# Optimization experiments

Hardware: AMD Instinct MI355X
Metric: run time of the kernel (lower is better)

Reference implementation:

```python
import jax, jax.numpy as jnp
import numpy as np

NEG = -1e30  # stand-in for -inf that keeps logaddexp grad-safe


def _ctc_neg_log_likelihood(predictions, labels):
    # predictions: [B, T, C] logits; labels: [B, L] int, -1 = padding.
    # tf.nn.ctc_loss(blank_index=-1) => blank class is C-1.
    B, T, C = predictions.shape
    L = labels.shape[1]
    S = 2 * L + 1
    blank = C - 1

    label_len = jnp.sum((labels != -1).astype(jnp.int32), axis=-1)  # [B]
    labels_c = jnp.where(labels < 0, 0, labels).astype(jnp.int32)

    # Extended label sequence: blank, l1, blank, l2, ..., blank  -> [B, S]
    ext = jnp.full((B, S), blank, dtype=jnp.int32)
    ext = ext.at[:, 1::2].set(labels_c)

    # s-2 transition allowed only at label positions (odd s) with ext[s] != ext[s-2]
    same = jnp.concatenate([jnp.zeros((B, 2), bool), ext[:, 2:] == ext[:, :-2]], axis=1)
    is_label_pos = (jnp.arange(S) % 2 == 1)[None, :]
    allow2 = is_label_pos & ~same  # [B, S]

    # valid extended positions per example: s < 2*label_len + 1
    valid = jnp.arange(S)[None, :] < (2 * label_len + 1)[:, None]  # [B, S]

    log_probs = jax.nn.log_softmax(predictions, axis=-1)  # [B, T, C]
    # emission log-prob for each extended-label slot: [B, T, S]
    lp_ext = jnp.take_along_axis(log_probs, jnp.broadcast_to(ext[:, None, :], (B, T, S)), axis=2)

    has_lab = label_len > 0
    alpha0 = jnp.full((B, S), NEG, dtype=log_probs.dtype)
    alpha0 = alpha0.at[:, 0].set(lp_ext[:, 0, 0])
    alpha0 = alpha0.at[:, 1].set(jnp.where(has_lab, lp_ext[:, 0, 1], NEG))
    alpha0 = jnp.where(valid, alpha0, NEG)

    def step(alpha, lp_t):
        a1 = alpha
        a2 = jnp.pad(alpha, ((0, 0), (1, 0)), constant_values=NEG)[:, :S]
        a3 = jnp.pad(alpha, ((0, 0), (2, 0)), constant_values=NEG)[:, :S]
        a3 = jnp.where(allow2, a3, NEG)
        new = jnp.logaddexp(jnp.logaddexp(a1, a2), a3) + lp_t
        new = jnp.where(valid, new, NEG)
        return new, None

    lp_rest = jnp.moveaxis(lp_ext[:, 1:], 1, 0)  # [T-1, B, S]
    alphaT, _ = jax.lax.scan(step, alpha0, lp_rest)

    idx1 = (2 * label_len)[:, None]              # final blank
    idx2 = jnp.maximum(idx1 - 1, 0)              # final label
    a_end1 = jnp.take_along_axis(alphaT, idx1, axis=1)[:, 0]
    a_end2 = jnp.take_along_axis(alphaT, idx2, axis=1)[:, 0]
    a_end2 = jnp.where(has_lab, a_end2, NEG)
    log_lik = jnp.logaddexp(a_end1, a_end2)
    return -log_lik  # [B]


def setup_inputs() -> dict:
    key = jax.random.key(0)
    k1, k2 = jax.random.split(key)
    B, T, C, L = 1024, 384, 96, 48
    labels = jax.random.randint(k1, (B, L), 0, C - 1).astype(jnp.int64)
    predictions = jax.random.normal(k2, (B, T, C), dtype=jnp.float32)
    return {"labels": labels, "predictions": predictions}


def reference(labels, predictions):
    per_example = _ctc_neg_log_likelihood(predictions, labels)
    return jnp.mean(per_example)
```

## Files before the change

kernel.cpp:

```cpp
#include <hip/hip_runtime.h>

constexpr int Tt = 384;
constexpr int Cc = 96;
constexpr int Ll = 48;
constexpr int Gg = 8;
constexpr int NG = 24;

#define L2E 1.4426950408889634f
#define LN2 0.6931471805599453f
#define LNEG (-3.0e38f)

template <int CTRL, int RM = 0xF>
__device__ __forceinline__ float dppf(float x) {
    return __int_as_float(
        __builtin_amdgcn_update_dpp(0, __float_as_int(x), CTRL, RM, 0xF, true));
}
template <int CTRL>
__device__ __forceinline__ int dppi(int x) {
    return __builtin_amdgcn_update_dpp(0, x, CTRL, 0xF, 0xF, true);
}
__device__ __forceinline__ float bcast63(float x) {
    return __int_as_float(__builtin_amdgcn_readlane(__float_as_int(x), 63));
}
__device__ __forceinline__ float wsum(float x) {
    x += dppf<0x111>(x);
    x += dppf<0x112>(x);
    x += dppf<0x114>(x);
    x += dppf<0x118>(x);
    x += dppf<0x142, 0xA>(x);
    x += dppf<0x143, 0xC>(x);
    return bcast63(x);
}
__device__ __forceinline__ float shup1(float x) { return dppf<0x138>(x); }
__device__ __forceinline__ float shdn1(float x) { return dppf<0x130>(x); }
__device__ __forceinline__ float exp2i(int d) {
    d = d < -126 ? -126 : (d > 126 ? 126 : d);
    return __int_as_float((d + 127) << 23);
}

template <bool FWD>
__device__ __forceinline__ void half_pass(const float2* __restrict__ rp2, int lane,
                                          int idx_h, int bitsel, float allow2f,
                                          float& st_e, float& st_o, int& ls) {
    float2 q[Gg];
    float pbC[Gg], plC[Gg], pbN[Gg], plN[Gg];

    auto loadg = [&](int g) {
#pragma unroll
        for (int j = 0; j < Gg; ++j) {
            int k = g * Gg + j;
            int t = FWD ? k : (Tt - 1 - k);
            q[j] = (lane < 48) ? rp2[(size_t)t * 48 + lane] : make_float2(-1e4f, -1e4f);
        }
    };
    auto emit = [&](float* pb, float* pl, int gnext) {
        float ex[Gg], ey[Gg], s[Gg], gb[Gg], g0[Gg], g1[Gg];
#pragma unroll
        for (int j = 0; j < Gg; ++j) {
            ex[j] = exp2f(q[j].x * L2E);
            ey[j] = exp2f(q[j].y * L2E);
            s[j]  = ex[j] + ey[j];
        }
#pragma unroll
        for (int j = 0; j < Gg; ++j) {
            gb[j] = __shfl(ey[j], 47, 64);
            g0[j] = __shfl(ex[j], idx_h, 64);
            g1[j] = __shfl(ey[j], idx_h, 64);
        }
        if (gnext < NG) loadg(gnext);
#pragma unroll
        for (int j = 0; j < Gg; ++j) s[j] = wsum(s[j]);
#pragma unroll
        for (int j = 0; j < Gg; ++j) {
            float rZ = __builtin_amdgcn_rcpf(s[j]);
            pb[j] = gb[j] * rZ;
            pl[j] = (bitsel ? g1[j] : g0[j]) * rZ;
        }
    };

    float f   = 1.0f;
    float a2f = allow2f;

    loadg(0);
    emit(pbC, plC, 1);

    for (int g = 0; g < NG; ++g) {
        if (g + 1 < NG) emit(pbN, plN, g + 2);
#pragma unroll
        for (int j = 0; j < Gg; ++j) {
            if (FWD) {
                float sh = shup1(st_o);
                float t0 = st_e + st_o;
                float ne = fmaf(f, sh, st_e) * pbC[j];
                float no = fmaf(a2f, sh, t0) * plC[j];
                st_e = ne; st_o = no;
            } else {
                float en = shdn1(st_e);
                float on = shdn1(st_o);
                float ne = (st_e + st_o) * pbC[j];
                float no = fmaf(a2f, on, fmaf(f, en, st_o)) * plC[j];
                st_e = ne; st_o = no;
            }
        }
        float m = fmaxf(st_e, st_o);
        bool z = (m == 0.0f);
        int eb = (__float_as_int(m) >> 23) & 0xFF;
        eb = eb > 253 ? 253 : eb;
        float r = z ? 1.0f : __int_as_float((254 - eb) << 23);
        st_e *= r; st_o *= r;
        ls += z ? 0 : (eb - 127);
#pragma unroll
        for (int it = 0; it < 8; ++it) {
            int lsn = FWD ? dppi<0x138>(ls) : dppi<0x130>(ls);
            ls = z ? lsn : ls;
        }
        int lsn2 = FWD ? dppi<0x138>(ls) : dppi<0x130>(ls);
        f = exp2i(lsn2 - ls);
        a2f = allow2f * f;
        if (g + 1 < NG) {
#pragma unroll
            for (int j = 0; j < Gg; ++j) { pbC[j] = pbN[j]; plC[j] = plN[j]; }
        }
    }
}

__global__ __launch_bounds__(64) void zero_kernel(float* o) { *o = 0.0f; }

__global__ __launch_bounds__(128) void ctc_fb(const int* __restrict__ labels,
                                              const float* __restrict__ pred,
                                              float* __restrict__ out,
                                              float invB) {
    const int b    = blockIdx.x;
    const int lane = threadIdx.x & 63;
    const int wv   = threadIdx.x >> 6;
    const float2* rp2 = (const float2*)(pred + (size_t)b * Tt * Cc);

    int v = (lane < Ll) ? labels[(size_t)b * Ll + lane] : -1;
    int present = (lane < Ll) && (v != -1);
    int labv = (v < 0) ? 0 : v;
    unsigned long long pm = __ballot(present);
    int len = __popcll(pm);

    int idx_h  = labv >> 1;
    int bitsel = labv & 1;
    int lab_p = __shfl(labv, (lane - 1) & 63, 64);
    int lab_n = __shfl(labv, (lane + 1) & 63, 64);

    __shared__ float sbe[64], sbo[64];
    __shared__ int   slsb[64];

    float Ae = 0.0f, Ao = 0.0f;
    int ls_f = 0;
    if (wv == 0) {
        float allow2f = (lane >= 1 && labv != lab_p) ? 1.0f : 0.0f;
        float a_e = (lane == 0) ? 1.0f : 0.0f;
        float a_o = 0.0f;
        half_pass<true>(rp2, lane, idx_h, bitsel, allow2f, a_e, a_o, ls_f);
        float sh  = shup1(a_o);
        int   lsu = dppi<0x138>(ls_f);
        float fup = exp2i(lsu - ls_f);
        Ae = fmaf(fup, sh, a_e);
        Ao = fmaf(allow2f * fup, sh, a_e + a_o);
    } else {
        float allow2f = (labv != lab_n) ? 1.0f : 0.0f;
        float b_e = (lane == len) ? 1.0f : 0.0f;
        float b_o = 0.0f;
        int ls_b = 0;
        half_pass<false>(rp2, lane, idx_h, bitsel, allow2f, b_e, b_o, ls_b);
        sbe[lane]  = b_e;
        sbo[lane]  = b_o;
        slsb[lane] = ls_b;
    }
    __syncthreads();

    if (wv == 0) {
        float be = sbe[lane], bo = sbo[lane];
        float base = (float)(ls_f + slsb[lane]);
        float l1 = (Ae > 0.0f && be > 0.0f) ? __log2f(Ae) + __log2f(be) + base : LNEG;
        float l2 = (Ao > 0.0f && bo > 0.0f) ? __log2f(Ao) + __log2f(bo) + base : LNEG;
        float mm = fmaxf(l1, l2);
#pragma unroll
        for (int off = 32; off >= 1; off >>= 1) mm = fmaxf(mm, __shfl_xor(mm, off, 64));
        float ss = exp2f(l1 - mm) + exp2f(l2 - mm);
#pragma unroll
        for (int off = 32; off >= 1; off >>= 1) ss += __shfl_xor(ss, off, 64);
        if (lane == 0) {
            float ll = (mm + __log2f(ss)) * LN2;
            atomicAdd(out, -ll * invB);
        }
    }
}

extern "C" void kernel_launch(void* const* d_in, const int* in_sizes, int n_in,
                              void* d_out, int out_size, void* d_ws, size_t ws_size,
                              hipStream_t stream) {
    const int*   labels = (const int*)d_in[0];
    const float* pred   = (const float*)d_in[1];
    float*       out    = (float*)d_out;

    const int B = in_sizes[0] / Ll;

    hipLaunchKernelGGL(zero_kernel, dim3(1), dim3(64), 0, stream, out);
    hipLaunchKernelGGL(ctc_fb, dim3(B), dim3(128), 0, stream,
                       labels, pred, out, 1.0f / (float)B);
}
```

Baseline: 227.2 us.

## Split emission softmax into separate kernel writing fp16 probs to workspace

Adds a preceding kernel that computes softmax-normalised emission probabilities for each extended-label slot with 8 waves per example, and stores them as fp16 into a [B,T,64] workspace. Lane 48 holds the blank probability. The recurrence kernel then only loads the precomputed halves with a four-group prefetch and broadcasts the blank value via readlane. This removes the exp/shuffle/reduction work from the serial recurrence critical path and cuts the bytes it reads. In exchange it adds a workspace round trip and a second launch, and fp16 storage of probabilities risks precision loss or underflow for small values.

Measured after the change: 248.1 us. 1.09x slower.

```diff
diff --git a/kernel.cpp b/kernel.cpp
--- a/kernel.cpp
+++ b/kernel.cpp
@@ -1,10 +1,12 @@
 #include <hip/hip_runtime.h>
+#include <hip/hip_fp16.h>
 
 constexpr int Tt = 384;
 constexpr int Cc = 96;
 constexpr int Ll = 48;
 constexpr int Gg = 8;
 constexpr int NG = 24;
+constexpr int ES = 64;
 
 #define L2E 1.4426950408889634f
 #define LN2 0.6931471805599453f
@@ -38,54 +40,83 @@
     return __int_as_float((d + 127) << 23);
 }
 
+__global__ __launch_bounds__(512) void emit_kernel(const int* __restrict__ labels,
+                                                   const float* __restrict__ pred,
+                                                   __half* __restrict__ em,
+                                                   float* __restrict__ out) {
+    const int b    = blockIdx.x;
+    const int lane = threadIdx.x & 63;
+    const int wv   = threadIdx.x >> 6;
+    if (b == 0 && threadIdx.x == 0) *out = 0.0f;
+
+    const float2* rp2  = (const float2*)(pred + (size_t)b * Tt * Cc);
+    __half*       erow = em + (size_t)b * Tt * ES;
+
+    int v = (lane < Ll) ? labels[(size_t)b * Ll + lane] : 0;
+    int labv   = (v < 0) ? 0 : v;
+    int idx_h  = labv >> 1;
+    int bitsel = labv & 1;
+
+    constexpr int U = 4;
+    for (int base = wv; base < Tt; base += 8 * U) {
+        float2 q[U];
+#pragma unroll
+        for (int u = 0; u < U; ++u) {
+            int t = base + 8 * u;
+            q[u] = (lane < 48) ? rp2[(size_t)t * 48 + lane] : make_float2(-1e4f, -1e4f);
+        }
+#pragma unroll
+        for (int u = 0; u < U; ++u) {
+            float ex = exp2f(q[u].x * L2E);
+            float ey = exp2f(q[u].y * L2E);
+            float s  = (lane < 48) ? (ex + ey) : 0.0f;
+            float gb = __shfl(ey, 47, 64);
+            float g0 = __shfl(ex, idx_h, 64);
+            float g1 = __shfl(ey, idx_h, 64);
+            s = wsum(s);
+            float rZ = __builtin_amdgcn_rcpf(s);
+            float pl = (bitsel ? g1 : g0) * rZ;
+            float pb = gb * rZ;
+            float val = (lane < 48) ? pl : pb;
+            int t = base + 8 * u;
+            erow[(size_t)t * ES + lane] = __float2half(val);
+        }
+    }
+}
+
 template <bool FWD>
-__device__ __forceinline__ void half_pass(const float2* __restrict__ rp2, int lane,
-                                          int idx_h, int bitsel, float allow2f,
-                                          float& st_e, float& st_o, int& ls) {
-    float2 q[Gg];
-    float pbC[Gg], plC[Gg], pbN[Gg], plN[Gg];
-
-    auto loadg = [&](int g) {
+__device__ __forceinline__ void half_pass(const __half* __restrict__ erow, int lane,
+                                          float allow2f, float& st_e, float& st_o, int& ls) {
+    __half qr[4][Gg];
+    float plC[Gg], pbC[Gg], plN[Gg], pbN[Gg];
+
+    auto loadg = [&](__half* dst, int g) {
 #pragma unroll
         for (int j = 0; j < Gg; ++j) {
             int k = g * Gg + j;
             int t = FWD ? k : (Tt - 1 - k);
-            q[j] = (lane < 48) ? rp2[(size_t)t * 48 + lane] : make_float2(-1e4f, -1e4f);
+            dst[j] = erow[(size_t)t * ES + lane];
         }
     };
-    auto emit = [&](float* pb, float* pl, int gnext) {
-        float ex[Gg], ey[Gg], s[Gg], gb[Gg], g0[Gg], g1[Gg];
+    auto conv = [&](const __half* src, float* pl, float* pb) {
 #pragma unroll
         for (int j = 0; j < Gg; ++j) {
-            ex[j] = exp2f(q[j].x * L2E);
-            ey[j] = exp2f(q[j].y * L2E);
-            s[j]  = ex[j] + ey[j];
-        }
-#pragma unroll
-        for (int j = 0; j < Gg; ++j) {
-            gb[j] = __shfl(ey[j], 47, 64);
-            g0[j] = __shfl(ex[j], idx_h, 64);
-            g1[j] = __shfl(ey[j], idx_h, 64);
-        }
-        if (gnext < NG) loadg(gnext);
-#pragma unroll
-        for (int j = 0; j < Gg; ++j) s[j] = wsum(s[j]);
-#pragma unroll
-        for (int j = 0; j < Gg; ++j) {
-            float rZ = __builtin_amdgcn_rcpf(s[j]);
-            pb[j] = gb[j] * rZ;
-            pl[j] = (bitsel ? g1[j] : g0[j]) * rZ;
+            float vf = __half2float(src[j]);
+            pl[j] = vf;
+            pb[j] = __int_as_float(__builtin_amdgcn_readlane(__float_as_int(vf), 48));
         }
     };
+
+    loadg(qr[0], 0); loadg(qr[1], 1); loadg(qr[2], 2); loadg(qr[3], 3);
+    conv(qr[0], plC, pbC);
 
     float f   = 1.0f;
     float a2f = allow2f;
 
-    loadg(0);
-    emit(pbC, plC, 1);
-
+#pragma unroll
     for (int g = 0; g < NG; ++g) {
-        if (g + 1 < NG) emit(pbN, plN, g + 2);
+        if (g + 1 < NG) conv(qr[(g + 1) & 3], plN, pbN);
+        if (g + 4 < NG) loadg(qr[g & 3], g + 4);
 #pragma unroll
         for (int j = 0; j < Gg; ++j) {
             if (FWD) {
@@ -103,8 +134,8 @@
             }
         }
         float m = fmaxf(st_e, st_o);
-        bool z = (m == 0.0f);
-        int eb = (__float_as_int(m) >> 23) & 0xFF;
+        bool z  = (m == 0.0f);
+        int eb  = (__float_as_int(m) >> 23) & 0xFF;
         eb = eb > 253 ? 253 : eb;
         float r = z ? 1.0f : __int_as_float((254 - eb) << 23);
         st_e *= r; st_o *= r;
@@ -115,25 +146,23 @@
             ls = z ? lsn : ls;
         }
         int lsn2 = FWD ? dppi<0x138>(ls) : dppi<0x130>(ls);
-        f = exp2i(lsn2 - ls);
+        f   = exp2i(lsn2 - ls);
         a2f = allow2f * f;
         if (g + 1 < NG) {
 #pragma unroll
-            for (int j = 0; j < Gg; ++j) { pbC[j] = pbN[j]; plC[j] = plN[j]; }
-        }
-    }
-}
-
-__global__ __launch_bounds__(64) void zero_kernel(float* o) { *o = 0.0f; }
-
-__global__ __launch_bounds__(128) void ctc_fb(const int* __restrict__ labels,
-                                              const float* __restrict__ pred,
-                                              float* __restrict__ out,
-                                              float invB) {
+            for (int j = 0; j < Gg; ++j) { plC[j] = plN[j]; pbC[j] = pbN[j]; }
+        }
+    }
+}
+
+__global__ __launch_bounds__(128) void ctc_fb2(const int* __restrict__ labels,
+                                               const __half* __restrict__ em,
+                                               float* __restrict__ out,
+                                               float invB) {
     const int b    = blockIdx.x;
     const int lane = threadIdx.x & 63;
     const int wv   = threadIdx.x >> 6;
-    const float2* rp2 = (const float2*)(pred + (size_t)b * Tt * Cc);
+    const __half* erow = em + (size_t)b * Tt * ES;
 
     int v = (lane < Ll) ? labels[(size_t)b * Ll + lane] : -1;
     int present = (lane < Ll) && (v != -1);
@@ -141,8 +170,6 @@
     unsigned long long pm = __ballot(present);
     int len = __popcll(pm);
 
-    int idx_h  = labv >> 1;
-    int bitsel = labv & 1;
     int lab_p = __shfl(labv, (lane - 1) & 63, 64);
     int lab_n = __shfl(labv, (lane + 1) & 63, 64);
 
@@ -155,7 +182,7 @@
         float allow2f = (lane >= 1 && labv != lab_p) ? 1.0f : 0.0f;
         float a_e = (lane == 0) ? 1.0f : 0.0f;
         float a_o = 0.0f;
-        half_pass<true>(rp2, lane, idx_h, bitsel, allow2f, a_e, a_o, ls_f);
+        half_pass<true>(erow, lane, allow2f, a_e, a_o, ls_f);
         float sh  = shup1(a_o);
         int   lsu = dppi<0x138>(ls_f);
         float fup = exp2i(lsu - ls_f);
@@ -166,7 +193,7 @@
         float b_e = (lane == len) ? 1.0f : 0.0f;
         float b_o = 0.0f;
         int ls_b = 0;
-        half_pass<false>(rp2, lane, idx_h, bitsel, allow2f, b_e, b_o, ls_b);
+        half_pass<false>(erow, lane, allow2f, b_e, b_o, ls_b);
         sbe[lane]  = b_e;
         sbo[lane]  = b_o;
         slsb[lane] = ls_b;
@@ -197,10 +224,10 @@
     const int*   labels = (const int*)d_in[0];
     const float* pred   = (const float*)d_in[1];
     float*       out    = (float*)d_out;
+    __half*      em     = (__half*)d_ws;
 
     const int B = in_sizes[0] / Ll;
 
-    hipLaunchKernelGGL(zero_kernel, dim3(1), dim3(64), 0, stream, out);
-    hipLaunchKernelGGL(ctc_fb, dim3(B), dim3(128), 0, stream,
-                       labels, pred, out, 1.0f / (float)B);
-}
+    hipLaunchKernelGGL(emit_kernel, dim3(B), dim3(512), 0, stream, labels, pred, em, out);
+    hipLaunchKernelGGL(ctc_fb2, dim3(B), dim3(128), 0, stream, labels, em, out, 1.0f / (float)B);
+}
```

## Split CTC forward-backward into producer and DP waves using LDS double buffering

Applied to the files above, without the earlier changes.

Splits the work per block across four waves instead of two. Two producer waves load logits and compute softmax-normalised emission probabilities into a double-buffered shared-memory ring, and two consumer waves run the forward and backward alpha/beta recurrences from LDS. The goal is to take the exp/shuffle/reduction work off the serial DP critical path so it overlaps with the recurrence. The cost is a __syncthreads per group, extra LDS traffic and twice the threads per block, which may reduce occupancy.

Result: no change. 226.1 us (-0.5%).

```diff
diff --git a/kernel.cpp b/kernel.cpp
--- a/kernel.cpp
+++ b/kernel.cpp
@@ -39,94 +39,79 @@
 }
 
 template <bool FWD>
-__device__ __forceinline__ void half_pass(const float2* __restrict__ rp2, int lane,
-                                          int idx_h, int bitsel, float allow2f,
-                                          float& st_e, float& st_o, int& ls) {
-    float2 q[Gg];
-    float pbC[Gg], plC[Gg], pbN[Gg], plN[Gg];
-
-    auto loadg = [&](int g) {
-#pragma unroll
-        for (int j = 0; j < Gg; ++j) {
-            int k = g * Gg + j;
-            int t = FWD ? k : (Tt - 1 - k);
-            q[j] = (lane < 48) ? rp2[(size_t)t * 48 + lane] : make_float2(-1e4f, -1e4f);
+__device__ __forceinline__ void prod_load(const float2* __restrict__ rp2, float2* q,
+                                          int g, int lane) {
+#pragma unroll
+    for (int j = 0; j < Gg; ++j) {
+        int k = g * Gg + j;
+        int t = FWD ? k : (Tt - 1 - k);
+        q[j] = (lane < 48) ? rp2[(size_t)t * 48 + lane] : make_float2(-1e4f, -1e4f);
+    }
+}
+__device__ __forceinline__ void prod_group(const float2* q, float* dst, int lane,
+                                           int idx_h, int bitsel) {
+#pragma unroll
+    for (int j = 0; j < Gg; ++j) {
+        float ex = exp2f(q[j].x * L2E);
+        float ey = exp2f(q[j].y * L2E);
+        float s  = (lane < 48) ? (ex + ey) : 0.0f;
+        float gb = __shfl(ey, 47, 64);
+        float g0 = __shfl(ex, idx_h, 64);
+        float g1 = __shfl(ey, idx_h, 64);
+        s = wsum(s);
+        float rZ = __builtin_amdgcn_rcpf(s);
+        float pl = (bitsel ? g1 : g0) * rZ;
+        float pb = gb * rZ;
+        dst[j * 64 + lane] = (lane == 49) ? pb : pl;
+    }
+}
+
+template <bool FWD>
+__device__ __forceinline__ void dp_group(const float* __restrict__ pr, int lane,
+                                         float allow2f, float& st_e, float& st_o,
+                                         int& ls, float& f, float& a2f) {
+    float plC[Gg], pbC[Gg];
+#pragma unroll
+    for (int j = 0; j < Gg; ++j) {
+        plC[j] = pr[j * 64 + lane];
+        pbC[j] = pr[j * 64 + 49];
+    }
+#pragma unroll
+    for (int j = 0; j < Gg; ++j) {
+        if (FWD) {
+            float sh = shup1(st_o);
+            float t0 = st_e + st_o;
+            float ne = fmaf(f, sh, st_e) * pbC[j];
+            float no = fmaf(a2f, sh, t0) * plC[j];
+            st_e = ne; st_o = no;
+        } else {
+            float en = shdn1(st_e);
+            float on = shdn1(st_o);
+            float ne = (st_e + st_o) * pbC[j];
+            float no = fmaf(a2f, on, fmaf(f, en, st_o)) * plC[j];
+            st_e = ne; st_o = no;
         }
-    };
-    auto emit = [&](float* pb, float* pl, int gnext) {
-        float ex[Gg], ey[Gg], s[Gg], gb[Gg], g0[Gg], g1[Gg];
-#pragma unroll
-        for (int j = 0; j < Gg; ++j) {
-            ex[j] = exp2f(q[j].x * L2E);
-            ey[j] = exp2f(q[j].y * L2E);
-            s[j]  = ex[j] + ey[j];
-        }
-#pragma unroll
-        for (int j = 0; j < Gg; ++j) {
-            gb[j] = __shfl(ey[j], 47, 64);
-            g0[j] = __shfl(ex[j], idx_h, 64);
-            g1[j] = __shfl(ey[j], idx_h, 64);
-        }
-        if (gnext < NG) loadg(gnext);
-#pragma unroll
-        for (int j = 0; j < Gg; ++j) s[j] = wsum(s[j]);
-#pragma unroll
-        for (int j = 0; j < Gg; ++j) {
-            float rZ = __builtin_amdgcn_rcpf(s[j]);
-            pb[j] = gb[j] * rZ;
-            pl[j] = (bitsel ? g1[j] : g0[j]) * rZ;
-        }
-    };
-
-    float f   = 1.0f;
-    float a2f = allow2f;
-
-    loadg(0);
-    emit(pbC, plC, 1);
-
-    for (int g = 0; g < NG; ++g) {
-        if (g + 1 < NG) emit(pbN, plN, g + 2);
-#pragma unroll
-        for (int j = 0; j < Gg; ++j) {
-            if (FWD) {
-                float sh = shup1(st_o);
-                float t0 = st_e + st_o;
-                float ne = fmaf(f, sh, st_e) * pbC[j];
-                float no = fmaf(a2f, sh, t0) * plC[j];
-                st_e = ne; st_o = no;
-            } else {
-                float en = shdn1(st_e);
-                float on = shdn1(st_o);
-                float ne = (st_e + st_o) * pbC[j];
-                float no = fmaf(a2f, on, fmaf(f, en, st_o)) * plC[j];
-                st_e = ne; st_o = no;
-            }
-        }
-        float m = fmaxf(st_e, st_o);
-        bool z = (m == 0.0f);
-        int eb = (__float_as_int(m) >> 23) & 0xFF;
-        eb = eb > 253 ? 253 : eb;
-        float r = z ? 1.0f : __int_as_float((254 - eb) << 23);
-        st_e *= r; st_o *= r;
-        ls += z ? 0 : (eb - 127);
-#pragma unroll
-        for (int it = 0; it < 8; ++it) {
-            int lsn = FWD ? dppi<0x138>(ls) : dppi<0x130>(ls);
-            ls = z ? lsn : ls;
-        }
-        int lsn2 = FWD ? dppi<0x138>(ls) : dppi<0x130>(ls);
-        f = exp2i(lsn2 - ls);
-        a2f = allow2f * f;
-        if (g + 1 < NG) {
-#pragma unroll
-            for (int j = 0; j < Gg; ++j) { pbC[j] = pbN[j]; plC[j] = plN[j]; }
-        }
-    }
+    }
+    float m = fmaxf(st_e, st_o);
+    bool z  = (m == 0.0f);
+    int eb  = (__float_as_int(m) >> 23) & 0xFF;
+    eb = eb > 253 ? 253 : eb;
+    float r = z ? 1.0f : __int_as_float((254 - eb) << 23);
+    st_e *= r; st_o *= r;
+    ls += z ? 0 : (eb - 127);
+#pragma unroll
+    for (int it = 0; it < 8; ++it) {
+        int lsn = FWD ? dppi<0x138>(ls) : dppi<0x130>(ls);
+        ls = z ? lsn : ls;
+    }
+    int lsn2 = FWD ? dppi<0x138>(ls) : dppi<0x130>(ls);
+    f   = exp2i(lsn2 - ls);
+    a2f = allow2f * f;
 }
 
 __global__ __launch_bounds__(64) void zero_kernel(float* o) { *o = 0.0f; }
 
-__global__ __launch_bounds__(128) void ctc_fb(const int* __restrict__ labels,
+__global__ __launch_bounds__(256) void ctc_fb(const int* __restrict__ labels,
                                               const float* __restrict__ pred,
                                               float* __restrict__ out,
                                               float invB) {
@@ -135,47 +120,80 @@
     const int wv   = threadIdx.x >> 6;
     const float2* rp2 = (const float2*)(pred + (size_t)b * Tt * Cc);
 
+    __shared__ float plb[2][2][Gg][64];
+    __shared__ float sbe[64], sbo[64];
+    __shared__ int   slsb[64];
+
     int v = (lane < Ll) ? labels[(size_t)b * Ll + lane] : -1;
     int present = (lane < Ll) && (v != -1);
     int labv = (v < 0) ? 0 : v;
     unsigned long long pm = __ballot(present);
     int len = __popcll(pm);
-
     int idx_h  = labv >> 1;
     int bitsel = labv & 1;
     int lab_p = __shfl(labv, (lane - 1) & 63, 64);
     int lab_n = __shfl(labv, (lane + 1) & 63, 64);
 
-    __shared__ float sbe[64], sbo[64];
-    __shared__ int   slsb[64];
-
-    float Ae = 0.0f, Ao = 0.0f;
-    int ls_f = 0;
+    float st_e = 0.0f, st_o = 0.0f, f = 1.0f, a2f = 0.0f, allow2f = 0.0f;
+    int   ls = 0;
+    float2 qA[Gg], qB[Gg];
+
     if (wv == 0) {
-        float allow2f = (lane >= 1 && labv != lab_p) ? 1.0f : 0.0f;
-        float a_e = (lane == 0) ? 1.0f : 0.0f;
-        float a_o = 0.0f;
-        half_pass<true>(rp2, lane, idx_h, bitsel, allow2f, a_e, a_o, ls_f);
-        float sh  = shup1(a_o);
-        int   lsu = dppi<0x138>(ls_f);
-        float fup = exp2i(lsu - ls_f);
-        Ae = fmaf(fup, sh, a_e);
-        Ao = fmaf(allow2f * fup, sh, a_e + a_o);
+        allow2f = (lane >= 1 && labv != lab_p) ? 1.0f : 0.0f;
+        st_e = (lane == 0) ? 1.0f : 0.0f;
+        a2f = allow2f;
+    } else if (wv == 1) {
+        allow2f = (labv != lab_n) ? 1.0f : 0.0f;
+        st_e = (lane == len) ? 1.0f : 0.0f;
+        a2f = allow2f;
+    } else if (wv == 2) {
+        prod_load<true>(rp2, qA, 0, lane);
+        prod_load<true>(rp2, qB, 1, lane);
     } else {
-        float allow2f = (labv != lab_n) ? 1.0f : 0.0f;
-        float b_e = (lane == len) ? 1.0f : 0.0f;
-        float b_o = 0.0f;
-        int ls_b = 0;
-        half_pass<false>(rp2, lane, idx_h, bitsel, allow2f, b_e, b_o, ls_b);
-        sbe[lane]  = b_e;
-        sbo[lane]  = b_o;
-        slsb[lane] = ls_b;
+        prod_load<false>(rp2, qA, 0, lane);
+        prod_load<false>(rp2, qB, 1, lane);
+    }
+
+    for (int i = 0; i <= NG; ++i) {
+        if (wv == 2 && i < NG) {
+            if ((i & 1) == 0) {
+                prod_group(qA, &plb[0][0][0][0], lane, idx_h, bitsel);
+                if (i + 2 < NG) prod_load<true>(rp2, qA, i + 2, lane);
+            } else {
+                prod_group(qB, &plb[0][1][0][0], lane, idx_h, bitsel);
+                if (i + 2 < NG) prod_load<true>(rp2, qB, i + 2, lane);
+            }
+        } else if (wv == 3 && i < NG) {
+            if ((i & 1) == 0) {
+                prod_group(qA, &plb[1][0][0][0], lane, idx_h, bitsel);
+                if (i + 2 < NG) prod_load<false>(rp2, qA, i + 2, lane);
+            } else {
+                prod_group(qB, &plb[1][1][0][0], lane, idx_h, bitsel);
+                if (i + 2 < NG) prod_load<false>(rp2, qB, i + 2, lane);
+            }
+        } else if (wv == 0 && i >= 1) {
+            dp_group<true>(&plb[0][(i - 1) & 1][0][0], lane, allow2f, st_e, st_o, ls, f, a2f);
+        } else if (wv == 1 && i >= 1) {
+            dp_group<false>(&plb[1][(i - 1) & 1][0][0], lane, allow2f, st_e, st_o, ls, f, a2f);
+        }
+        __syncthreads();
+    }
+
+    if (wv == 1) {
+        sbe[lane]  = st_e;
+        sbo[lane]  = st_o;
+        slsb[lane] = ls;
     }
     __syncthreads();
 
     if (wv == 0) {
+        float sh  = shup1(st_o);
+        int   lsu = dppi<0x138>(ls);
+        float fup = exp2i(lsu - ls);
+        float Ae = fmaf(fup, sh, st_e);
+        float Ao = fmaf(allow2f * fup, sh, st_e + st_o);
         float be = sbe[lane], bo = sbo[lane];
-        float base = (float)(ls_f + slsb[lane]);
+        float base = (float)(ls + slsb[lane]);
         float l1 = (Ae > 0.0f && be > 0.0f) ? __log2f(Ae) + __log2f(be) + base : LNEG;
         float l2 = (Ao > 0.0f && bo > 0.0f) ? __log2f(Ao) + __log2f(bo) + base : LNEG;
         float mm = fmaxf(l1, l2);
@@ -201,6 +219,6 @@
     const int B = in_sizes[0] / Ll;
 
     hipLaunchKernelGGL(zero_kernel, dim3(1), dim3(64), 0, stream, out);
-    hipLaunchKernelGGL(ctc_fb, dim3(B), dim3(128), 0, stream,
+    hipLaunchKernelGGL(ctc_fb, dim3(B), dim3(256), 0, stream,
                        labels, pred, out, 1.0f / (float)B);
 }
```
